# Kernel optimization log

Hardware: AMD Instinct MI355X
Metric: run time of the kernel (lower is better)

Reference implementation:

```python
import jax, jax.numpy as jnp
import numpy as np

EPSILON = 1e-8
B, T, H = 4, 4096, 2048          # batch, seq, hidden_dim
D, NH, K = 256, 4, 32            # belief_dim, num_heads, top_k
NB, NG = 65536, 16               # n_beliefs, n_goals
NEG_INF = -1e30


def setup_inputs() -> dict:
    key = jax.random.key(0)
    ks = jax.random.split(key, 8)
    hidden = jax.random.normal(ks[0], (B, T, H), dtype=jnp.float32)
    beliefs = jax.random.normal(ks[1], (NB, D), dtype=jnp.float32)
    active_mask = jax.random.bernoulli(ks[2], 0.5, (NB,))
    goal_embeddings = jax.random.normal(ks[3], (NG, D), dtype=jnp.float32)
    goal_priorities = jax.random.uniform(ks[4], (NG,), dtype=jnp.float32)
    # torch nn.Linear weights are [out_features, in_features]
    Wq = jax.random.normal(ks[5], (NH * D, H), dtype=jnp.float32) / np.float32(np.sqrt(H))
    Wo = jax.random.normal(ks[6], (H, NH * D), dtype=jnp.float32) / np.float32(np.sqrt(NH * D))
    log_temperature = jax.random.normal(ks[7], (NH,), dtype=jnp.float32) * 0.1
    return {"hidden": hidden, "beliefs": beliefs, "active_mask": active_mask,
            "goal_embeddings": goal_embeddings, "goal_priorities": goal_priorities,
            "Wq": Wq, "Wo": Wo, "log_temperature": log_temperature}


def reference(hidden, beliefs, active_mask, goal_embeddings, goal_priorities, Wq, Wo, log_temperature):
    # --- rough-score top-k pre-filter over active beliefs (N_active > top_k path) ---
    mean_query = hidden.mean(axis=(0, 1))                      # [H]
    rough_query = (Wq @ mean_query).reshape(NH, D).mean(axis=0)  # [D]
    radii = jnp.maximum(jnp.linalg.norm(beliefs, axis=-1), EPSILON)  # [NB]
    angles = beliefs / radii[:, None]                          # [NB, D]
    rough_scores = angles @ rough_query                        # [NB]
    # mask-gather: inactive beliefs get -inf so topk selects only active ones
    rough_scores = jnp.where(active_mask, rough_scores, NEG_INF)
    _, topk_idx = jax.lax.top_k(rough_scores, K)               # [K]
    active_beliefs = beliefs[topk_idx]                         # [K, D]

    # --- angle-normalized keys, raw values ---
    a_radii = jnp.maximum(jnp.linalg.norm(active_beliefs, axis=-1), EPSILON)
    keys = active_beliefs / a_radii[:, None]                   # [K, D]
    values = active_beliefs                                    # [K, D]

    # --- per-head queries and temperature ---
    queries = (hidden @ Wq.T).reshape(B, T, NH, D)             # [B,T,h,D]
    temperature = jnp.maximum(jnp.exp(log_temperature), 0.1)   # [h]
    scores = jnp.einsum('bthd,nd->bthn', queries, keys) / np.float32(np.sqrt(D))
    scores = scores * temperature[None, None, :, None]         # [B,T,h,K]

    # --- goal-similarity bias ---
    g_radii = jnp.maximum(jnp.linalg.norm(goal_embeddings, axis=-1), EPSILON)
    goal_angles = goal_embeddings / g_radii[:, None]           # [NG, D]
    sim = (keys @ goal_angles.T) * goal_priorities[None, :]    # [K, NG]
    goal_bias = sim.max(axis=-1)                               # [K], same for all heads
    scores = scores + goal_bias[None, None, None, :]

    attn = jax.nn.softmax(scores, axis=-1)                     # [B,T,h,K]
    retrieved = jnp.einsum('bthn,nd->bthd', attn, values).reshape(B, T, NH * D)
    return retrieved @ Wo.T                                    # [B,T,H]
```

## Files before the change

### kernel.cpp

```cpp
#include <hip/hip_runtime.h>

typedef unsigned int u32;
typedef unsigned short u16;
typedef unsigned long long u64;

typedef __bf16 bf16x8 __attribute__((ext_vector_type(8)));
typedef float f32x4 __attribute__((ext_vector_type(4)));

#define DEV __device__ __forceinline__

DEV u16 f2bf(float f) {
  u32 u = __float_as_uint(f);
  u += 0x7fffu + ((u >> 16) & 1u);
  return (u16)(u >> 16);
}
DEV float bf2f(u16 u) { return __uint_as_float((u32)u << 16); }

DEV void gld_lds16(const void* g, void* l) {
  __builtin_amdgcn_global_load_lds((const __attribute__((address_space(1))) u32*)g,
                                   (__attribute__((address_space(3))) u32*)l, 16, 0, 0);
}

DEV u64 packkey(float f, u32 idx) {
  u32 u = __float_as_uint(f);
  u = (u & 0x80000000u) ? ~u : (u | 0x80000000u);
  return ((u64)u << 32) | (u32)(~idx);
}

__global__ __launch_bounds__(256) void k_conv_mean(const float4* __restrict__ hidden4,
                                                   ushort4* __restrict__ hb4,
                                                   float4* __restrict__ partial4) {
  const int c4 = blockIdx.x * 256 + threadIdx.x;
  const int r0 = blockIdx.y * 64;
  float4 s = {0.f, 0.f, 0.f, 0.f};
  for (int r = 0; r < 64; r++) {
    float4 v = hidden4[(size_t)(r0 + r) * 512 + c4];
    ushort4 o; o.x = f2bf(v.x); o.y = f2bf(v.y); o.z = f2bf(v.z); o.w = f2bf(v.w);
    hb4[(size_t)(r0 + r) * 512 + c4] = o;
    s.x += v.x; s.y += v.y; s.z += v.z; s.w += v.w;
  }
  partial4[blockIdx.y * 512 + c4] = s;
}

__global__ __launch_bounds__(256) void k_mean(const float* __restrict__ partial,
                                              float* __restrict__ mean) {
  __shared__ float red[256];
  const int t = threadIdx.x;
  const int c = t & 15, s = t >> 4;
  const int col = blockIdx.x * 16 + c;
  float acc = 0.f;
  for (int ch = s; ch < 256; ch += 16) acc += partial[ch * 2048 + col];
  red[t] = acc;
  __syncthreads();
  for (int st = 8; st > 0; st >>= 1) {
    if (s < st) red[t] += red[t + st * 16];
    __syncthreads();
  }
  if (s == 0) mean[col] = red[c] * (1.0f / 16384.0f);
}

__global__ __launch_bounds__(256) void k_rq(const float* __restrict__ Wq,
                                            const float* __restrict__ mean,
                                            float* __restrict__ rq) {
  const int w = threadIdx.x >> 6, l = threadIdx.x & 63;
  const int row = blockIdx.x * 4 + w;
  float s = 0.f;
#pragma unroll
  for (int j = 0; j < 32; j++)
    s = fmaf(Wq[(size_t)row * 2048 + j * 64 + l], mean[j * 64 + l], s);
  for (int mk = 1; mk < 64; mk <<= 1) s += __shfl_xor(s, mk);
  if (l == 0) atomicAdd(&rq[row & 255], 0.25f * s);
}

__global__ __launch_bounds__(256) void k_rough(const float* __restrict__ beliefs,
                                               const void* __restrict__ amask,
                                               const float* __restrict__ rq,
                                               u64* __restrict__ keys) {
  const int t = threadIdx.x, w = t >> 6, l = t & 63;
  const int n = blockIdx.x * 4 + w;
  u32 mv = ((const u32*)amask)[l];
  bool isInt = (__ballot(mv > 1u) == 0ull);
  float4 b = *(const float4*)(beliefs + (size_t)n * 256 + l * 4);
  float4 qv = *(const float4*)(rq + l * 4);
  float dot = b.x * qv.x + b.y * qv.y + b.z * qv.z + b.w * qv.w;
  float ss = b.x * b.x + b.y * b.y + b.z * b.z + b.w * b.w;
  for (int mk = 1; mk < 64; mk <<= 1) { dot += __shfl_xor(dot, mk); ss += __shfl_xor(ss, mk); }
  if (l == 0) {
    bool act = isInt ? (((const int*)amask)[n] != 0)
                     : (((const unsigned char*)amask)[n] != 0);
    float score = act ? dot / fmaxf(sqrtf(ss), 1e-8f) : -1e30f;
    keys[n] = packkey(score, (u32)n);
  }
}

__global__ __launch_bounds__(256) void k_top1(const u64* __restrict__ keys,
                                              u64* __restrict__ cands) {
  __shared__ u64 ws[128];
  const int t = threadIdx.x, w = t >> 6, l = t & 63;
  const u64* src = keys + (size_t)blockIdx.x * 1024;
  u64 v0 = src[t], v1 = src[t + 256], v2 = src[t + 512], v3 = src[t + 768];
  for (int r = 0; r < 32; r++) {
    u64 a = v0 > v1 ? v0 : v1;
    u64 b = v2 > v3 ? v2 : v3;
    u64 m = a > b ? a : b;
#pragma unroll
    for (int mk = 1; mk < 64; mk <<= 1) { u64 o = __shfl_xor(m, mk); m = o > m ? o : m; }
    if (l == 0) ws[w * 32 + r] = m;
    v0 = (v0 == m) ? 0ull : v0;
    v1 = (v1 == m) ? 0ull : v1;
    v2 = (v2 == m) ? 0ull : v2;
    v3 = (v3 == m) ? 0ull : v3;
  }
  __syncthreads();
  if (w == 0) {
    u64 u0 = ws[l], u1 = ws[64 + l];
    for (int r = 0; r < 32; r++) {
      u64 m = u0 > u1 ? u0 : u1;
#pragma unroll
      for (int mk = 1; mk < 64; mk <<= 1) { u64 o = __shfl_xor(m, mk); m = o > m ? o : m; }
      if (l == 0) cands[blockIdx.x * 32 + r] = m;
      u0 = (u0 == m) ? 0ull : u0;
      u1 = (u1 == m) ? 0ull : u1;
    }
  }
}

__global__ __launch_bounds__(256) void k_top2_prep(const u64* __restrict__ cands,
                                                   const float* __restrict__ beliefs,
                                                   const float* __restrict__ goals,
                                                   const float* __restrict__ prio,
                                                   const float* __restrict__ logt,
                                                   float* __restrict__ keysf_g,
                                                   float* __restrict__ valsf_g,
                                                   float* __restrict__ biasO,
                                                   float* __restrict__ tempO) {
  __shared__ u64 ws[128];
  __shared__ int idxS[32];
  __shared__ float keysf[32 * 256];
  __shared__ float gradS[16];
  const int t = threadIdx.x, w = t >> 6, l = t & 63;
  u64 v[8];
#pragma unroll
  for (int i = 0; i < 8; i++) v[i] = cands[t + i * 256];
  for (int r = 0; r < 32; r++) {
    u64 m = v[0];
#pragma unroll
    for (int i = 1; i < 8; i++) m = v[i] > m ? v[i] : m;
#pragma unroll
    for (int mk = 1; mk < 64; mk <<= 1) { u64 o = __shfl_xor(m, mk); m = o > m ? o : m; }
    if (l == 0) ws[w * 32 + r] = m;
#pragma unroll
    for (int i = 0; i < 8; i++) v[i] = (v[i] == m) ? 0ull : v[i];
  }
  __syncthreads();
  if (w == 0) {
    u64 u0 = ws[l], u1 = ws[64 + l];
    for (int r = 0; r < 32; r++) {
      u64 m = u0 > u1 ? u0 : u1;
#pragma unroll
      for (int mk = 1; mk < 64; mk <<= 1) { u64 o = __shfl_xor(m, mk); m = o > m ? o : m; }
      if (l == 0) idxS[r] = (int)(~(u32)(m & 0xffffffffull));
      u0 = (u0 == m) ? 0ull : u0;
      u1 = (u1 == m) ? 0ull : u1;
    }
  }
  __syncthreads();
  for (int g = w * 4; g < w * 4 + 4; g++) {
    float4 gv = *(const float4*)(goals + g * 256 + l * 4);
    float ss = gv.x * gv.x + gv.y * gv.y + gv.z * gv.z + gv.w * gv.w;
    for (int mk = 1; mk < 64; mk <<= 1) ss += __shfl_xor(ss, mk);
    if (l == 0) gradS[g] = fmaxf(sqrtf(ss), 1e-8f);
  }
  for (int kk = w * 8; kk < w * 8 + 8; kk++) {
    int idx = idxS[kk];
    float4 bv = *(const float4*)(beliefs + (size_t)idx * 256 + l * 4);
    float ss = bv.x * bv.x + bv.y * bv.y + bv.z * bv.z + bv.w * bv.w;
    for (int mk = 1; mk < 64; mk <<= 1) ss += __shfl_xor(ss, mk);
    float rr = 1.0f / fmaxf(sqrtf(ss), 1e-8f);
    float4 kv; kv.x = bv.x * rr; kv.y = bv.y * rr; kv.z = bv.z * rr; kv.w = bv.w * rr;
    *(float4*)&keysf[kk * 256 + l * 4] = kv;
    *(float4*)&keysf_g[kk * 256 + l * 4] = kv;
    *(float4*)&valsf_g[kk * 256 + l * 4] = bv;
  }
  __syncthreads();
  for (int kk = w * 8; kk < w * 8 + 8; kk++) {
    float4 kv = *(const float4*)&keysf[kk * 256 + l * 4];
    float best = -1e30f;
    for (int g = 0; g < 16; g++) {
      float4 gv = *(const float4*)(goals + g * 256 + l * 4);
      float d = kv.x * gv.x + kv.y * gv.y + kv.z * gv.z + kv.w * gv.w;
      for (int mk = 1; mk < 64; mk <<= 1) d += __shfl_xor(d, mk);
      float sim = d / gradS[g] * prio[g];
      best = fmaxf(best, sim);
    }
    if (l == 0) biasO[kk] = best;
  }
  if (t < 4) tempO[t] = fmaxf(__expf(logt[t]), 0.1f);
}

__global__ __launch_bounds__(256) void k_build(const float* __restrict__ Wq,
                                               const float* __restrict__ Wo,
                                               const float* __restrict__ keysf_g,
                                               const float* __restrict__ valsf_g,
                                               u16* __restrict__ Kp,
                                               u16* __restrict__ VWoT) {
  __shared__ __align__(16) float sbuf[16384];
  const int t = threadIdx.x;
  if (blockIdx.x < 128) {
    float* keysS = sbuf;
    float* WqS = sbuf + 8192;
    const int h = blockIdx.x >> 5;
    const int c0 = (blockIdx.x & 31) * 64;
#pragma unroll
    for (int it = 0; it < 32; it++) keysS[t + it * 256] = keysf_g[t + it * 256];
    const int n0 = (t >> 5) * 4;
    const int c2 = (t & 31) * 2;
    float acc[4][2] = {};
    for (int dc = 0; dc < 4; dc++) {
      __syncthreads();
#pragma unroll
      for (int it = 0; it < 16; it++) {
        int i = t + it * 256;
        int r = i >> 6, c = i & 63;
        WqS[i] = Wq[(size_t)(h * 256 + dc * 64 + r) * 2048 + c0 + c];
      }
      __syncthreads();
      for (int d4 = 0; d4 < 16; d4++) {
        float4 kv[4];
#pragma unroll
        for (int i = 0; i < 4; i++)
          kv[i] = *(const float4*)&keysS[(n0 + i) * 256 + dc * 64 + d4 * 4];
#pragma unroll
        for (int dd = 0; dd < 4; dd++) {
          float2 w2 = *(const float2*)&WqS[(d4 * 4 + dd) * 64 + c2];
          float kvd[4] = {kv[0][dd], kv[1][dd], kv[2][dd], kv[3][dd]};
#pragma unroll
          for (int i = 0; i < 4; i++) {
            acc[i][0] = fmaf(kvd[i], w2.x, acc[i][0]);
            acc[i][1] = fmaf(kvd[i], w2.y, acc[i][1]);
          }
        }
      }
    }
#pragma unroll
    for (int i = 0; i < 4; i++) {
      u32 pk = (u32)f2bf(acc[i][0]) | ((u32)f2bf(acc[i][1]) << 16);
      *(u32*)&Kp[(size_t)(h * 32 + n0 + i) * 2048 + c0 + c2] = pk;
    }
  } else {
    float* valsS = sbuf;
    float* WoS = sbuf + 8192;
    const int c0 = (blockIdx.x - 128) * 32;
#pragma unroll
    for (int it = 0; it < 32; it++) valsS[t + it * 256] = valsf_g[t + it * 256];
    const int c = t >> 3;
    const int n0 = (t & 7) * 4;
    for (int h = 0; h < 4; h++) {
      __syncthreads();
#pragma unroll
      for (int it = 0; it < 32; it++) {
        int i = t + it * 256;
        int r = i >> 8, d = i & 255;
        WoS[i] = Wo[(size_t)(c0 + r) * 1024 + h * 256 + d];
      }
      __syncthreads();
      float acc[4] = {};
      for (int d4 = 0; d4 < 64; d4++) {
        float4 w4 = *(const float4*)&WoS[c * 256 + d4 * 4];
#pragma unroll
        for (int i = 0; i < 4; i++) {
          float4 kv = *(const float4*)&valsS[(n0 + i) * 256 + d4 * 4];
          acc[i] = fmaf(w4.x, kv.x, acc[i]);
          acc[i] = fmaf(w4.y, kv.y, acc[i]);
          acc[i] = fmaf(w4.z, kv.z, acc[i]);
          acc[i] = fmaf(w4.w, kv.w, acc[i]);
        }
      }
      ushort4 o; o.x = f2bf(acc[0]); o.y = f2bf(acc[1]); o.z = f2bf(acc[2]); o.w = f2bf(acc[3]);
      *(ushort4*)&VWoT[(size_t)(c0 + c) * 128 + h * 32 + n0] = o;
    }
  }
}

__global__ __launch_bounds__(512) void k_attn(const u16* __restrict__ hb,
                                              const u16* __restrict__ kp,
                                              const u16* __restrict__ vwot,
                                              const float* __restrict__ bias,
                                              const float* __restrict__ temp,
                                              float* __restrict__ out) {
  __shared__ __align__(16) u16 smem[57344];
  u16* Plds = smem + 49152;
  const int t = threadIdx.x;
  const int w = t >> 6, l = t & 63;
  const int q = l >> 4, c = l & 15;
  const int m0 = blockIdx.x * 64;
  const int rh = w >> 2, hd = w & 3;

  const float ts = temp[hd] * 0.0625f;
  const float b0 = bias[c], b1 = bias[16 + c];
  asm volatile("s_waitcnt vmcnt(0) lgkmcnt(0)" ::: "memory");

  const int rowA = t >> 3;
  const int cbA = (t & 7) ^ (rowA & 7);
  const u16* srcA = hb + (size_t)(m0 + rowA) * 2048 + cbA * 8;
  const int rowB1 = 64 + rowA;
  const int cbB0 = (t & 7) ^ (rowA & 7);
  const int cbB1 = (t & 7) ^ (rowB1 & 7);
  const u16* srcB0 = kp + (size_t)rowA * 2048 + cbB0 * 8;
  const u16* srcB1 = kp + (size_t)rowB1 * 2048 + cbB1 * 8;
  u16* dstA = smem + w * 512;
  u16* dstB0 = smem + 16384 + w * 512;
  u16* dstB1 = smem + 16384 + 4096 + w * 512;

  auto issue3 = [&](int j) {
    const int bo = j & 3;
    gld_lds16(srcA + j * 64, dstA + bo * 4096);
    gld_lds16(srcB0 + j * 64, dstB0 + bo * 8192);
    gld_lds16(srcB1 + j * 64, dstB1 + bo * 8192);
  };

  f32x4 acc[2][2] = {};
  issue3(0); issue3(1); issue3(2);

  for (int s = 0; s < 32; s++) {
    if (s <= 29)      asm volatile("s_waitcnt vmcnt(6)" ::: "memory");
    else if (s == 30) asm volatile("s_waitcnt vmcnt(3)" ::: "memory");
    else              asm volatile("s_waitcnt vmcnt(0)" ::: "memory");
    __builtin_amdgcn_s_barrier();
    __builtin_amdgcn_sched_barrier(0);
    if (s < 29) issue3(s + 3);

    const u16* Ab = smem + (s & 3) * 4096;
    const u16* Bb = smem + 16384 + (s & 3) * 8192;
    bf16x8 af[2][2], bfr[2][2];
#pragma unroll
    for (int mi = 0; mi < 2; mi++) {
      const int ra = rh * 32 + mi * 16 + c;
#pragma unroll
      for (int ks = 0; ks < 2; ks++)
        af[mi][ks] = __builtin_bit_cast(bf16x8,
            *(const uint4*)&Ab[ra * 64 + (((ks * 4 + q) ^ (ra & 7)) * 8)]);
    }
#pragma unroll
    for (int ni = 0; ni < 2; ni++) {
      const int rb = hd * 32 + ni * 16 + c;
#pragma unroll
      for (int ks = 0; ks < 2; ks++)
        bfr[ni][ks] = __builtin_bit_cast(bf16x8,
            *(const uint4*)&Bb[rb * 64 + (((ks * 4 + q) ^ (rb & 7)) * 8)]);
    }
    asm volatile("s_waitcnt lgkmcnt(0)" ::: "memory");
    __builtin_amdgcn_sched_barrier(0);
#pragma unroll
    for (int ks = 0; ks < 2; ks++)
#pragma unroll
      for (int mi = 0; mi < 2; mi++)
#pragma unroll
        for (int ni = 0; ni < 2; ni++)
          acc[mi][ni] = __builtin_amdgcn_mfma_f32_16x16x32_bf16(af[mi][ks], bfr[ni][ks],
                                                                acc[mi][ni], 0, 0, 0);
  }

#pragma unroll
  for (int mi = 0; mi < 2; mi++) {
#pragma unroll
    for (int r = 0; r < 4; r++) {
      float v0 = fmaf(acc[mi][0][r], ts, b0);
      float v1 = fmaf(acc[mi][1][r], ts, b1);
      float m = fmaxf(v0, v1);
#pragma unroll
      for (int mk = 1; mk <= 8; mk <<= 1) m = fmaxf(m, __shfl_xor(m, mk));
      float e0 = __expf(v0 - m), e1 = __expf(v1 - m);
      float sum = e0 + e1;
#pragma unroll
      for (int mk = 1; mk <= 8; mk <<= 1) sum += __shfl_xor(sum, mk);
      float inv = 1.0f / sum;
      const int rp = rh * 32 + mi * 16 + q * 4 + r;
      const int k0 = hd * 32 + c, k1 = k0 + 16;
      Plds[rp * 128 + (((k0 >> 3) ^ (rp & 7)) * 8) + (k0 & 7)] = f2bf(e0 * inv);
      Plds[rp * 128 + (((k1 >> 3) ^ (rp & 7)) * 8) + (k1 & 7)] = f2bf(e1 * inv);
    }
  }
  __syncthreads();

  const int col0 = w * 256;
  bf16x8 pa[4][4];
#pragma unroll
  for (int mi = 0; mi < 4; mi++) {
    const int rp = mi * 16 + c;
#pragma unroll
    for (int ks = 0; ks < 4; ks++)
      pa[mi][ks] = __builtin_bit_cast(bf16x8,
          *(const uint4*)&Plds[rp * 128 + (((ks * 4 + q) ^ (rp & 7)) * 8)]);
  }
#pragma unroll
  for (int ni = 0; ni < 16; ni++) {
    const int rv = col0 + ni * 16 + c;
    const u16* vr = vwot + (size_t)rv * 128 + q * 8;
    bf16x8 vb[4];
#pragma unroll
    for (int ks = 0; ks < 4; ks++)
      vb[ks] = __builtin_bit_cast(bf16x8, *(const uint4*)(vr + ks * 32));
    f32x4 oacc[4] = {};
#pragma unroll
    for (int mi = 0; mi < 4; mi++)
#pragma unroll
      for (int ks = 0; ks < 4; ks++)
        oacc[mi] = __builtin_amdgcn_mfma_f32_16x16x32_bf16(pa[mi][ks], vb[ks], oacc[mi], 0, 0, 0);
    const int col = col0 + ni * 16 + c;
#pragma unroll
    for (int mi = 0; mi < 4; mi++)
#pragma unroll
      for (int r = 0; r < 4; r++)
        out[(size_t)(m0 + mi * 16 + q * 4 + r) * 2048 + col] = oacc[mi][r];
  }
}

extern "C" void kernel_launch(void* const* d_in, const int* in_sizes, int n_in,
                              void* d_out, int out_size, void* d_ws, size_t ws_size,
                              hipStream_t stream) {
  const float* hidden = (const float*)d_in[0];
  const float* beliefs = (const float*)d_in[1];
  const void* amask = d_in[2];
  const float* goals = (const float*)d_in[3];
  const float* prio = (const float*)d_in[4];
  const float* Wq = (const float*)d_in[5];
  const float* Wo = (const float*)d_in[6];
  const float* logt = (const float*)d_in[7];
  float* out = (float*)d_out;

  char* ws = (char*)d_ws;
  size_t off = 0;
  auto alloc = [&](size_t bytes) { char* p = ws + off; off = (off + bytes + 255) & ~(size_t)255; return p; };
  u16* hb      = (u16*)alloc(67108864);
  u16* kp      = (u16*)alloc(524288);
  u16* vwot    = (u16*)alloc(524288);
  float* partial = (float*)alloc(2097152);
  float* meanq = (float*)alloc(8192);
  float* rq    = (float*)alloc(1024);
  u64* keys    = (u64*)alloc(524288);
  u64* cands   = (u64*)alloc(16384);
  float* keysf = (float*)alloc(32768);
  float* valsf = (float*)alloc(32768);
  float* biasv = (float*)alloc(128);
  float* tempv = (float*)alloc(16);

  hipMemsetAsync(rq, 0, 1024, stream);
  k_conv_mean<<<dim3(2, 256), 256, 0, stream>>>((const float4*)hidden, (ushort4*)hb, (float4*)partial);
  k_mean<<<128, 256, 0, stream>>>(partial, meanq);
  k_rq<<<256, 256, 0, stream>>>(Wq, meanq, rq);
  k_rough<<<16384, 256, 0, stream>>>(beliefs, amask, rq, keys);
  k_top1<<<64, 256, 0, stream>>>(keys, cands);
  k_top2_prep<<<1, 256, 0, stream>>>(cands, beliefs, goals, prio, logt, keysf, valsf, biasv, tempv);
  k_build<<<192, 256, 0, stream>>>(Wq, Wo, keysf, valsf, kp, vwot);
  k_attn<<<256, 512, 0, stream>>>(hb, kp, vwot, biasv, tempv, out);
}
```

Before: 505.2 us.

## Split conversion and attention kernels into smaller blocks for more parallelism

k_conv_mean now processes 16 rows per block instead of 64, launching four times as many blocks, and the partial-sum buffer and reduction loop grow to match. k_attn shrinks from 64-row, 512-thread tiles to 32-row, 256-thread tiles with a triple-buffered rather than quad-buffered LDS pipeline, so 512 blocks are launched and LDS use per block drops. The aim is better occupancy and load balance across the CUs. In exchange, each block reloads the full key-projection (kp) tile for only 32 rows, doubling kp traffic, and the mean reduction reads more partial sums.

```diff
diff --git a/kernel.cpp b/kernel.cpp
--- a/kernel.cpp
+++ b/kernel.cpp
@@ -31,9 +31,9 @@
                                                    ushort4* __restrict__ hb4,
                                                    float4* __restrict__ partial4) {
   const int c4 = blockIdx.x * 256 + threadIdx.x;
-  const int r0 = blockIdx.y * 64;
+  const int r0 = blockIdx.y * 16;
   float4 s = {0.f, 0.f, 0.f, 0.f};
-  for (int r = 0; r < 64; r++) {
+  for (int r = 0; r < 16; r++) {
     float4 v = hidden4[(size_t)(r0 + r) * 512 + c4];
     ushort4 o; o.x = f2bf(v.x); o.y = f2bf(v.y); o.z = f2bf(v.z); o.w = f2bf(v.w);
     hb4[(size_t)(r0 + r) * 512 + c4] = o;
@@ -49,7 +49,7 @@
   const int c = t & 15, s = t >> 4;
   const int col = blockIdx.x * 16 + c;
   float acc = 0.f;
-  for (int ch = s; ch < 256; ch += 16) acc += partial[ch * 2048 + col];
+  for (int ch = s; ch < 1024; ch += 16) acc += partial[ch * 2048 + col];
   red[t] = acc;
   __syncthreads();
   for (int st = 8; st > 0; st >>= 1) {
@@ -282,60 +282,66 @@
   }
 }
 
-__global__ __launch_bounds__(512) void k_attn(const u16* __restrict__ hb,
+__global__ __launch_bounds__(256) void k_attn(const u16* __restrict__ hb,
                                               const u16* __restrict__ kp,
                                               const u16* __restrict__ vwot,
                                               const float* __restrict__ bias,
                                               const float* __restrict__ temp,
                                               float* __restrict__ out) {
-  __shared__ __align__(16) u16 smem[57344];
-  u16* Plds = smem + 49152;
+  __shared__ __align__(16) u16 smem[34816];
+  u16* Plds = smem + 30720;
   const int t = threadIdx.x;
   const int w = t >> 6, l = t & 63;
   const int q = l >> 4, c = l & 15;
-  const int m0 = blockIdx.x * 64;
-  const int rh = w >> 2, hd = w & 3;
+  const int m0 = blockIdx.x * 32;
+  const int hd = w;
 
   const float ts = temp[hd] * 0.0625f;
   const float b0 = bias[c], b1 = bias[16 + c];
   asm volatile("s_waitcnt vmcnt(0) lgkmcnt(0)" ::: "memory");
 
   const int rowA = t >> 3;
-  const int cbA = (t & 7) ^ (rowA & 7);
-  const u16* srcA = hb + (size_t)(m0 + rowA) * 2048 + cbA * 8;
-  const int rowB1 = 64 + rowA;
-  const int cbB0 = (t & 7) ^ (rowA & 7);
-  const int cbB1 = (t & 7) ^ (rowB1 & 7);
-  const u16* srcB0 = kp + (size_t)rowA * 2048 + cbB0 * 8;
-  const u16* srcB1 = kp + (size_t)rowB1 * 2048 + cbB1 * 8;
+  const int slA = t & 7;
+  const u16* srcA = hb + (size_t)(m0 + rowA) * 2048 + (slA ^ (rowA & 7)) * 8;
   u16* dstA = smem + w * 512;
-  u16* dstB0 = smem + 16384 + w * 512;
-  u16* dstB1 = smem + 16384 + 4096 + w * 512;
-
-  auto issue3 = [&](int j) {
-    const int bo = j & 3;
-    gld_lds16(srcA + j * 64, dstA + bo * 4096);
-    gld_lds16(srcB0 + j * 64, dstB0 + bo * 8192);
-    gld_lds16(srcB1 + j * 64, dstB1 + bo * 8192);
+
+  const int lr = l >> 3, sl = l & 7;
+  const u16* srcB[4];
+#pragma unroll
+  for (int j = 0; j < 4; j++) {
+    const int rB = w * 32 + j * 8 + lr;
+    srcB[j] = kp + (size_t)rB * 2048 + (sl ^ (rB & 7)) * 8;
+  }
+  u16* dstB = smem + 6144 + w * 2048;
+
+  auto issue = [&](int sI, int bo) {
+    const int kt = sI * 64;
+    gld_lds16(srcA + kt, dstA + bo * 2048);
+#pragma unroll
+    for (int j = 0; j < 4; j++)
+      gld_lds16(srcB[j] + kt, dstB + bo * 8192 + j * 512);
   };
 
   f32x4 acc[2][2] = {};
-  issue3(0); issue3(1); issue3(2);
-
+  issue(0, 0); issue(1, 1);
+
+  int bo = 0;
   for (int s = 0; s < 32; s++) {
-    if (s <= 29)      asm volatile("s_waitcnt vmcnt(6)" ::: "memory");
-    else if (s == 30) asm volatile("s_waitcnt vmcnt(3)" ::: "memory");
-    else              asm volatile("s_waitcnt vmcnt(0)" ::: "memory");
+    if (s < 31) asm volatile("s_waitcnt vmcnt(5)" ::: "memory");
+    else        asm volatile("s_waitcnt vmcnt(0)" ::: "memory");
     __builtin_amdgcn_s_barrier();
     __builtin_amdgcn_sched_barrier(0);
-    if (s < 29) issue3(s + 3);
-
-    const u16* Ab = smem + (s & 3) * 4096;
-    const u16* Bb = smem + 16384 + (s & 3) * 8192;
+    if (s < 30) {
+      int bt = bo + 2; if (bt >= 3) bt -= 3;
+      issue(s + 2, bt);
+    }
+
+    const u16* Ab = smem + bo * 2048;
+    const u16* Bb = smem + 6144 + bo * 8192;
     bf16x8 af[2][2], bfr[2][2];
 #pragma unroll
     for (int mi = 0; mi < 2; mi++) {
-      const int ra = rh * 32 + mi * 16 + c;
+      const int ra = mi * 16 + c;
 #pragma unroll
       for (int ks = 0; ks < 2; ks++)
         af[mi][ks] = __builtin_bit_cast(bf16x8,
@@ -359,6 +365,7 @@
         for (int ni = 0; ni < 2; ni++)
           acc[mi][ni] = __builtin_amdgcn_mfma_f32_16x16x32_bf16(af[mi][ks], bfr[ni][ks],
                                                                 acc[mi][ni], 0, 0, 0);
+    bo = (bo + 1 == 3) ? 0 : bo + 1;
   }
 
 #pragma unroll
@@ -375,7 +382,7 @@
 #pragma unroll
       for (int mk = 1; mk <= 8; mk <<= 1) sum += __shfl_xor(sum, mk);
       float inv = 1.0f / sum;
-      const int rp = rh * 32 + mi * 16 + q * 4 + r;
+      const int rp = mi * 16 + q * 4 + r;
       const int k0 = hd * 32 + c, k1 = k0 + 16;
       Plds[rp * 128 + (((k0 >> 3) ^ (rp & 7)) * 8) + (k0 & 7)] = f2bf(e0 * inv);
       Plds[rp * 128 + (((k1 >> 3) ^ (rp & 7)) * 8) + (k1 & 7)] = f2bf(e1 * inv);
@@ -383,33 +390,33 @@
   }
   __syncthreads();
 
-  const int col0 = w * 256;
-  bf16x8 pa[4][4];
-#pragma unroll
-  for (int mi = 0; mi < 4; mi++) {
+  const int col0 = w * 512;
+  bf16x8 pa[2][4];
+#pragma unroll
+  for (int mi = 0; mi < 2; mi++) {
     const int rp = mi * 16 + c;
 #pragma unroll
     for (int ks = 0; ks < 4; ks++)
       pa[mi][ks] = __builtin_bit_cast(bf16x8,
           *(const uint4*)&Plds[rp * 128 + (((ks * 4 + q) ^ (rp & 7)) * 8)]);
   }
-#pragma unroll
-  for (int ni = 0; ni < 16; ni++) {
+#pragma unroll 2
+  for (int ni = 0; ni < 32; ni++) {
     const int rv = col0 + ni * 16 + c;
     const u16* vr = vwot + (size_t)rv * 128 + q * 8;
     bf16x8 vb[4];
 #pragma unroll
     for (int ks = 0; ks < 4; ks++)
       vb[ks] = __builtin_bit_cast(bf16x8, *(const uint4*)(vr + ks * 32));
-    f32x4 oacc[4] = {};
-#pragma unroll
-    for (int mi = 0; mi < 4; mi++)
+    f32x4 oacc[2] = {};
+#pragma unroll
+    for (int mi = 0; mi < 2; mi++)
 #pragma unroll
       for (int ks = 0; ks < 4; ks++)
         oacc[mi] = __builtin_amdgcn_mfma_f32_16x16x32_bf16(pa[mi][ks], vb[ks], oacc[mi], 0, 0, 0);
     const int col = col0 + ni * 16 + c;
 #pragma unroll
-    for (int mi = 0; mi < 4; mi++)
+    for (int mi = 0; mi < 2; mi++)
 #pragma unroll
       for (int r = 0; r < 4; r++)
         out[(size_t)(m0 + mi * 16 + q * 4 + r) * 2048 + col] = oacc[mi][r];
@@ -435,7 +442,7 @@
   u16* hb      = (u16*)alloc(67108864);
   u16* kp      = (u16*)alloc(524288);
   u16* vwot    = (u16*)alloc(524288);
-  float* partial = (float*)alloc(2097152);
+  float* partial = (float*)alloc(8388608);
   float* meanq = (float*)alloc(8192);
   float* rq    = (float*)alloc(1024);
   u64* keys    = (u64*)alloc(524288);
@@ -446,12 +453,12 @@
   float* tempv = (float*)alloc(16);
 
   hipMemsetAsync(rq, 0, 1024, stream);
-  k_conv_mean<<<dim3(2, 256), 256, 0, stream>>>((const float4*)hidden, (ushort4*)hb, (float4*)partial);
+  k_conv_mean<<<dim3(2, 1024), 256, 0, stream>>>((const float4*)hidden, (ushort4*)hb, (float4*)partial);
   k_mean<<<128, 256, 0, stream>>>(partial, meanq);
   k_rq<<<256, 256, 0, stream>>>(Wq, meanq, rq);
   k_rough<<<16384, 256, 0, stream>>>(beliefs, amask, rq, keys);
   k_top1<<<64, 256, 0, stream>>>(keys, cands);
   k_top2_prep<<<1, 256, 0, stream>>>(cands, beliefs, goals, prio, logt, keysf, valsf, biasv, tempv);
   k_build<<<192, 256, 0, stream>>>(Wq, Wo, keysf, valsf, kp, vwot);
-  k_attn<<<256, 512, 0, stream>>>(hb, kp, vwot, biasv, tempv, out);
-}
+  k_attn<<<512, 256, 0, stream>>>(hb, kp, vwot, biasv, tempv, out);
+}
```

New measurement: 521.9 us. +3.3%, slower.
